# Optimization experiments

Measured on AMD Instinct MI355X. Metric: run time of the kernel, lower is better.

Reference implementation:

```python
import jax, jax.numpy as jnp
import numpy as np

B, L, C, H = 2, 4096, 512, 8
DH = C // H


def setup_inputs() -> dict:
    key = jax.random.key(0)
    ks = jax.random.split(key, 6)
    s = 1.0 / np.sqrt(C)
    return {
        "x": jax.random.normal(ks[0], (B, L, C), dtype=jnp.float32),
        "Wq": jax.random.normal(ks[1], (C, C), dtype=jnp.float32) * s,
        "Wk": jax.random.normal(ks[2], (C, C), dtype=jnp.float32) * s,
        "Wv": jax.random.normal(ks[3], (C, C), dtype=jnp.float32) * s,
        "Wo": jax.random.normal(ks[4], (C, C), dtype=jnp.float32) * s,
        "bo": jnp.zeros((C,), dtype=jnp.float32),
    }


def reference(x, Wq, Wk, Wv, Wo, bo):
    # x: [B, L, C]; split heads -> [B, H, L, Dh]
    def heads(t):
        return t.reshape(B, L, H, DH).transpose(0, 2, 1, 3)

    q = heads(x @ Wq)
    k = heads(x @ Wk)
    v = heads(x @ Wv)
    scale = 1.0 / np.sqrt(DH)
    scores = jnp.einsum("bhqd,bhkd->bhqk", q, k) * scale  # [B,H,L,L]
    w = jax.nn.softmax(scores, axis=-1)  # dropout_rate=0.0 -> identity
    att = jnp.einsum("bhqk,bhkd->bhqd", w, v)  # [B,H,L,Dh]
    att = att.transpose(0, 2, 1, 3).reshape(B, L, C)
    return att @ Wo + bo
```

## Files before the change

kernel.cpp:

```cpp
#include <hip/hip_runtime.h>
#include <hip/hip_bf16.h>

typedef __hip_bfloat16 bh;
typedef __attribute__((ext_vector_type(8))) __bf16 bf16x8;
typedef __attribute__((ext_vector_type(4))) float f32x4;
typedef __attribute__((ext_vector_type(4))) int i32x4;
typedef __attribute__((ext_vector_type(4))) short s16x4;

#define NB 2
#define NL 4096
#define NC 512
#define NH 8
#define NDH 64
#define NM (NB * NL)
#define LOG2E 1.4426950408889634f
#define KVBLK 8192

static __device__ __forceinline__ f32x4 mfma_bf16(bf16x8 a, bf16x8 b, f32x4 c) {
    return __builtin_amdgcn_mfma_f32_16x16x32_bf16(a, b, c, 0, 0, 0);
}
static __device__ __forceinline__ f32x4 mfma16(s16x4 a, s16x4 b, f32x4 c) {
    return __builtin_amdgcn_mfma_f32_16x16x16bf16_1k(a, b, c, 0, 0, 0);
}

static __device__ __forceinline__ void st_bf4(bh* dst, float a, float b, float c, float d) {
    bh tmp[4] = {__float2bfloat16(a), __float2bfloat16(b),
                 __float2bfloat16(c), __float2bfloat16(d)};
    *(s16x4*)dst = *(const s16x4*)tmp;
}
static __device__ __forceinline__ s16x4 pk_bf4(float a, float b, float c, float d) {
    bh tmp[4] = {__float2bfloat16(a), __float2bfloat16(b),
                 __float2bfloat16(c), __float2bfloat16(d)};
    return *(const s16x4*)tmp;
}

static __device__ __forceinline__ void gload16(const bh* g, bh* l) {
    __builtin_amdgcn_global_load_lds(
        (const __attribute__((address_space(1))) void*)g,
        (__attribute__((address_space(3))) void*)l,
        16, 0, 0);
}

__global__ __launch_bounds__(256, 2)
void prep(const float* __restrict__ x,
          const float* __restrict__ Wq, const float* __restrict__ Wk,
          const float* __restrict__ Wv, const float* __restrict__ Wo,
          bh* __restrict__ xf, bh* __restrict__ Wf)
{
    const int t = threadIdx.x;
    const int wave = t >> 6, lane = t & 63;
    const int quad = lane >> 4, c16 = lane & 15;

    if (blockIdx.z < 8) {
        __shared__ __align__(16) bh T[64][72];
        const int m64 = blockIdx.x, k64 = blockIdx.z;
        #pragma unroll
        for (int rep = 0; rep < 4; rep++) {
            int li = t + rep * 256;
            int r = li >> 4, c4 = (li & 15) * 4;
            float4 f = *(const float4*)&x[(size_t)(m64 * 64 + r) * 512 + k64 * 64 + c4];
            st_bf4(&T[r][c4], f.x, f.y, f.z, f.w);
        }
        __syncthreads();
        #pragma unroll
        for (int kcl = 0; kcl < 2; kcl++) {
            i32x4 v = *(const i32x4*)&T[wave * 16 + c16][kcl * 32 + quad * 8];
            size_t addr = ((size_t)(m64 * 4 + wave) * 16 + (k64 * 2 + kcl)) * 512 + lane * 8;
            *(i32x4*)&xf[addr] = v;
        }
    } else {
        if (blockIdx.x >= 64) return;
        int task = blockIdx.x * 4 + wave;
        int z = task >> 6, nt = (task >> 3) & 7, k0i = task & 7;
        const float* W = (z == 0) ? Wq : (z == 1) ? Wk : (z == 2) ? Wv : Wo;
        bh* dst = Wf + (((size_t)z * 8 + nt) * 8 + k0i) * 4096;
        #pragma unroll
        for (int kc = 0; kc < 2; kc++)
            #pragma unroll
            for (int fn = 0; fn < 4; fn++) {
                bh tmp[8];
                #pragma unroll
                for (int j = 0; j < 8; j++)
                    tmp[j] = __float2bfloat16(
                        W[(size_t)(k0i * 64 + kc * 32 + quad * 8 + j) * 512
                          + nt * 64 + fn * 16 + c16]);
                *(i32x4*)&dst[(kc * 4 + fn) * 512 + lane * 8] = *(const i32x4*)tmp;
            }
    }
}

__global__ __launch_bounds__(256, 2)
void qkv_gemm(const bh* __restrict__ xf, const bh* __restrict__ Wf,
              bh* __restrict__ Qb, bh* __restrict__ KVf)
{
    __shared__ __align__(16) bh smem[2][20480];

    const int t = threadIdx.x;
    const int wave = t >> 6, lane = t & 63;
    const int quad = lane >> 4, c16 = lane & 15;
    const int m0 = blockIdx.x * 128;
    const int nt = blockIdx.y;
    const int m16b = m0 >> 4;

    f32x4 acc[3][2][4];
    for (int z = 0; z < 3; z++)
        for (int a = 0; a < 2; a++)
            for (int b = 0; b < 4; b++)
                for (int u = 0; u < 4; u++) acc[z][a][b][u] = 0.0f;

    auto stage = [&](int k0i, int buf) {
        bh* Xl = &smem[buf][0];
        bh* Wl = &smem[buf][8192];
        #pragma unroll
        for (int r = 0; r < 4; r++) {
            int f = wave * 4 + r;
            const bh* src = xf + ((size_t)(m16b + (f >> 1)) * 16 + k0i * 2 + (f & 1)) * 512
                          + lane * 8;
            gload16(src, &Xl[f * 512 + lane * 8]);
        }
        #pragma unroll
        for (int z = 0; z < 3; z++) {
            const bh* wz = Wf + (((size_t)z * 8 + nt) * 8 + k0i) * 4096;
            #pragma unroll
            for (int r = 0; r < 2; r++) {
                int off = (wave * 2 + r) * 512 + lane * 8;
                gload16(wz + off, &Wl[z * 4096 + off]);
            }
        }
    };

    stage(0, 0);
    for (int k0i = 0; k0i < 8; k0i++) {
        const int buf = k0i & 1;
        __syncthreads();
        if (k0i < 7) stage(k0i + 1, buf ^ 1);
        const bh* Xl = &smem[buf][0];
        const bh* Wl = &smem[buf][8192];
        #pragma unroll
        for (int kc = 0; kc < 2; kc++) {
            bf16x8 af0 = *(const bf16x8*)&Xl[((wave * 2 + 0) * 2 + kc) * 512 + lane * 8];
            bf16x8 af1 = *(const bf16x8*)&Xl[((wave * 2 + 1) * 2 + kc) * 512 + lane * 8];
            #pragma unroll
            for (int z = 0; z < 3; z++)
                #pragma unroll
                for (int fn = 0; fn < 4; fn++) {
                    bf16x8 bf = *(const bf16x8*)&Wl[z * 4096 + (kc * 4 + fn) * 512 + lane * 8];
                    acc[z][0][fn] = mfma_bf16(af0, bf, acc[z][0][fn]);
                    acc[z][1][fn] = mfma_bf16(af1, bf, acc[z][1][fn]);
                }
        }
        __syncthreads();
    }

    const int h = nt;
    const int b = m0 >> 12;
    const int l0 = m0 & 4095;
    const int bh_i = b * NH + h;
    const int kt0 = l0 >> 6;

    {
        bh* Tq = &smem[0][0];
        #pragma unroll
        for (int fm = 0; fm < 2; fm++)
            #pragma unroll
            for (int i = 0; i < 4; i++) {
                int ll = wave * 32 + fm * 16 + quad * 4 + i;
                #pragma unroll
                for (int fn = 0; fn < 4; fn++)
                    Tq[ll * 68 + fn * 16 + c16] =
                        __float2bfloat16(acc[0][fm][fn][i] * 0.125f);
            }
        __syncthreads();
        int l = t >> 1, half = t & 1;
        bh* dst = Qb + ((size_t)bh_i * NL + l0 + l) * NDH + half * 32;
        const bh* src = &Tq[l * 68 + half * 32];
        #pragma unroll
        for (int r = 0; r < 4; r++)
            *(i32x4*)(dst + r * 8) = *(const i32x4*)(src + r * 8);
        __syncthreads();
    }

    {
        bh* Tk = &smem[0][0];
        #pragma unroll
        for (int fm = 0; fm < 2; fm++)
            #pragma unroll
            for (int i = 0; i < 4; i++) {
                int ll = wave * 32 + fm * 16 + quad * 4 + i;
                int ktl = ll >> 6, l64 = ll & 63;
                int fk = l64 >> 4, c16t = l64 & 15;
                #pragma unroll
                for (int fn = 0; fn < 4; fn++) {
                    int d = fn * 16 + c16;
                    int kc = d >> 5, qt = (d >> 3) & 3, j = d & 7;
                    Tk[ktl * 4096 + (fk * 2 + kc) * 512 + (qt * 16 + c16t) * 8 + j] =
                        __float2bfloat16(acc[1][fm][fn][i] * LOG2E);
                }
            }
        __syncthreads();
        int idx = t * 32;
        int ktl = idx >> 12, wi = idx & 4095;
        bh* dst = KVf + (size_t)(bh_i * 64 + kt0 + ktl) * KVBLK + wi;
        #pragma unroll
        for (int r = 0; r < 4; r++)
            *(i32x4*)(dst + r * 8) = *(const i32x4*)&Tk[idx + r * 8];
    }

    #pragma unroll
    for (int fm = 0; fm < 2; fm++) {
        int fkv = (wave * 2 + fm) & 3;
        int ktv = kt0 + (wave >> 1);
        #pragma unroll
        for (int fn = 0; fn < 4; fn++) {
            size_t addr = (size_t)(bh_i * 64 + ktv) * KVBLK + 4096
                        + (size_t)(fn * 4 + fkv) * 256 + (quad * 16 + c16) * 4;
            st_bf4(&KVf[addr], acc[2][fm][fn][0], acc[2][fm][fn][1],
                               acc[2][fm][fn][2], acc[2][fm][fn][3]);
        }
    }
}

__global__ __launch_bounds__(512, 4)
void flash_attn(const bh* __restrict__ Qb, const bh* __restrict__ KVf,
                bh* __restrict__ attb)
{
    __shared__ __align__(16) bh SF[2][2][KVBLK];

    const int t = threadIdx.x;
    const int wave = t >> 6, lane = t & 63;
    const int group = wave >> 2, w4 = wave & 3;
    const int quad = lane >> 4, c16 = lane & 15;
    const int bh_idx = blockIdx.y;
    const int q0 = blockIdx.x * 128;

    const bh* Qp  = Qb + (size_t)bh_idx * NL * NDH;
    const bh* KVp = KVf + (size_t)bh_idx * 64 * KVBLK;

    bf16x8 qf[2][2];
    #pragma unroll
    for (int fq = 0; fq < 2; fq++)
        #pragma unroll
        for (int kc = 0; kc < 2; kc++)
            qf[fq][kc] = *(const bf16x8*)
                &Qp[(size_t)(q0 + w4 * 32 + fq * 16 + c16) * NDH + kc * 32 + quad * 8];

    f32x4 ot[4][2];
    float lsum[2] = {0.0f, 0.0f};
    for (int a = 0; a < 4; a++)
        for (int fq = 0; fq < 2; fq++)
            for (int u = 0; u < 4; u++) ot[a][fq][u] = 0.0f;
    const f32x4 z4 = {0.0f, 0.0f, 0.0f, 0.0f};

    auto stage = [&](int i, int buf) {
        int kt = 2 * i + group;
        #pragma unroll
        for (int r = 0; r < 4; r++) {
            int off = (w4 * 4 + r) * 512 + lane * 8;
            gload16(KVp + (size_t)kt * KVBLK + off, &SF[group][buf][off]);
        }
    };

    stage(0, 0);
    for (int i = 0; i < 32; i++) {
        const int buf = i & 1;
        __syncthreads();
        if (i < 31) stage(i + 1, buf ^ 1);
        const bh* sf = &SF[group][buf][0];

        f32x4 s[4][2];
        #pragma unroll
        for (int fk = 0; fk < 4; fk++) {
            bf16x8 kf0 = *(const bf16x8*)&sf[(fk * 2 + 0) * 512 + lane * 8];
            s[fk][0] = mfma_bf16(kf0, qf[0][0], z4);
            s[fk][1] = mfma_bf16(kf0, qf[1][0], z4);
        }
        #pragma unroll
        for (int fk = 0; fk < 4; fk++) {
            bf16x8 kf1 = *(const bf16x8*)&sf[(fk * 2 + 1) * 512 + lane * 8];
            s[fk][0] = mfma_bf16(kf1, qf[0][1], s[fk][0]);
            s[fk][1] = mfma_bf16(kf1, qf[1][1], s[fk][1]);
        }

        s16x4 vt[4][4];
        #pragma unroll
        for (int fn = 0; fn < 4; fn++)
            #pragma unroll
            for (int fk = 0; fk < 4; fk++)
                vt[fn][fk] = *(const s16x4*)&sf[4096 + (fn * 4 + fk) * 256 + lane * 4];

        s16x4 pf[4][2];
        float rs0 = 0.0f, rs1 = 0.0f;
        #pragma unroll
        for (int fk = 0; fk < 4; fk++) {
            float a0 = __builtin_amdgcn_exp2f(s[fk][0][0]);
            float a1 = __builtin_amdgcn_exp2f(s[fk][0][1]);
            float a2 = __builtin_amdgcn_exp2f(s[fk][0][2]);
            float a3 = __builtin_amdgcn_exp2f(s[fk][0][3]);
            rs0 += (a0 + a1) + (a2 + a3);
            pf[fk][0] = pk_bf4(a0, a1, a2, a3);
            float b0 = __builtin_amdgcn_exp2f(s[fk][1][0]);
            float b1 = __builtin_amdgcn_exp2f(s[fk][1][1]);
            float b2 = __builtin_amdgcn_exp2f(s[fk][1][2]);
            float b3 = __builtin_amdgcn_exp2f(s[fk][1][3]);
            rs1 += (b0 + b1) + (b2 + b3);
            pf[fk][1] = pk_bf4(b0, b1, b2, b3);
        }
        lsum[0] += rs0;
        lsum[1] += rs1;

        #pragma unroll
        for (int fk = 0; fk < 4; fk++)
            #pragma unroll
            for (int fn = 0; fn < 4; fn++) {
                ot[fn][0] = mfma16(vt[fn][fk], pf[fk][0], ot[fn][0]);
                ot[fn][1] = mfma16(vt[fn][fk], pf[fk][1], ot[fn][1]);
            }
    }

    #pragma unroll
    for (int fq = 0; fq < 2; fq++) {
        lsum[fq] += __shfl_xor(lsum[fq], 16);
        lsum[fq] += __shfl_xor(lsum[fq], 32);
    }

    float* Ocmb = (float*)&SF[0][0][0];
    float* Lcmb = Ocmb + 128 * 64;
    __syncthreads();
    if (group == 1) {
        #pragma unroll
        for (int fq = 0; fq < 2; fq++) {
            int q = w4 * 32 + fq * 16 + c16;
            #pragma unroll
            for (int fn = 0; fn < 4; fn++)
                *(f32x4*)&Ocmb[q * 64 + fn * 16 + quad * 4] = ot[fn][fq];
            if (quad == 0) Lcmb[q] = lsum[fq];
        }
    }
    __syncthreads();
    if (group == 0) {
        const int b = bh_idx >> 3, h = bh_idx & 7;
        const int mbase16 = (b * NL + q0) >> 4;
        #pragma unroll
        for (int fq = 0; fq < 2; fq++) {
            int q = w4 * 32 + fq * 16 + c16;
            float inv = 1.0f / (lsum[fq] + Lcmb[q]);
            int m16 = mbase16 + w4 * 2 + fq;
            #pragma unroll
            for (int fn = 0; fn < 4; fn++) {
                f32x4 o2 = *(const f32x4*)&Ocmb[q * 64 + fn * 16 + quad * 4];
                size_t addr = ((size_t)m16 * 16 + h * 2 + (fn >> 1)) * 512
                            + (size_t)(((fn & 1) * 2 + (quad >> 1)) * 16 + c16) * 8
                            + (quad & 1) * 4;
                st_bf4(&attb[addr],
                       (ot[fn][fq][0] + o2[0]) * inv, (ot[fn][fq][1] + o2[1]) * inv,
                       (ot[fn][fq][2] + o2[2]) * inv, (ot[fn][fq][3] + o2[3]) * inv);
            }
        }
    }
}

__global__ __launch_bounds__(256, 2)
void out_gemm(const bh* __restrict__ Af, const bh* __restrict__ Wf,
              const float* __restrict__ bo, float* __restrict__ out)
{
    __shared__ __align__(16) bh smem[2][12288];

    const int t = threadIdx.x;
    const int wave = t >> 6, lane = t & 63;
    const int quad = lane >> 4, c16 = lane & 15;
    const int m0 = blockIdx.x * 128;
    const int nt = blockIdx.y;
    const int n0 = nt * 64;
    const int m16b = m0 >> 4;

    f32x4 acc[2][4];
    for (int a = 0; a < 2; a++)
        for (int b = 0; b < 4; b++)
            for (int u = 0; u < 4; u++) acc[a][b][u] = 0.0f;

    auto stage = [&](int k0i, int buf) {
        bh* Xl = &smem[buf][0];
        bh* Wl = &smem[buf][8192];
        #pragma unroll
        for (int r = 0; r < 4; r++) {
            int f = wave * 4 + r;
            const bh* src = Af + ((size_t)(m16b + (f >> 1)) * 16 + k0i * 2 + (f & 1)) * 512
                          + lane * 8;
            gload16(src, &Xl[f * 512 + lane * 8]);
        }
        const bh* wz = Wf + (((size_t)3 * 8 + nt) * 8 + k0i) * 4096;
        #pragma unroll
        for (int r = 0; r < 2; r++) {
            int off = (wave * 2 + r) * 512 + lane * 8;
            gload16(wz + off, &Wl[off]);
        }
    };

    stage(0, 0);
    for (int k0i = 0; k0i < 8; k0i++) {
        const int buf = k0i & 1;
        __syncthreads();
        if (k0i < 7) stage(k0i + 1, buf ^ 1);
        const bh* Xl = &smem[buf][0];
        const bh* Wl = &smem[buf][8192];
        #pragma unroll
        for (int kc = 0; kc < 2; kc++) {
            bf16x8 af0 = *(const bf16x8*)&Xl[((wave * 2 + 0) * 2 + kc) * 512 + lane * 8];
            bf16x8 af1 = *(const bf16x8*)&Xl[((wave * 2 + 1) * 2 + kc) * 512 + lane * 8];
            #pragma unroll
            for (int fn = 0; fn < 4; fn++) {
                bf16x8 bf = *(const bf16x8*)&Wl[(kc * 4 + fn) * 512 + lane * 8];
                acc[0][fn] = mfma_bf16(af0, bf, acc[0][fn]);
                acc[1][fn] = mfma_bf16(af1, bf, acc[1][fn]);
            }
        }
        __syncthreads();
    }

    #pragma unroll
    for (int fm = 0; fm < 2; fm++)
        #pragma unroll
        for (int i = 0; i < 4; i++) {
            int mr = m0 + wave * 32 + fm * 16 + quad * 4 + i;
            #pragma unroll
            for (int fn = 0; fn < 4; fn++) {
                int cn = n0 + fn * 16 + c16;
                out[(size_t)mr * 512 + cn] = acc[fm][fn][i] + bo[cn];
            }
        }
}

extern "C" void kernel_launch(void* const* d_in, const int* in_sizes, int n_in,
                              void* d_out, int out_size, void* d_ws, size_t ws_size,
                              hipStream_t stream)
{
    const float* x  = (const float*)d_in[0];
    const float* Wq = (const float*)d_in[1];
    const float* Wk = (const float*)d_in[2];
    const float* Wv = (const float*)d_in[3];
    const float* Wo = (const float*)d_in[4];
    const float* bo = (const float*)d_in[5];
    float* out = (float*)d_out;

    const size_t mat = (size_t)NM * NC;
    bh* Qb   = (bh*)d_ws;
    bh* KVf  = Qb + mat;
    bh* attb = KVf + 2 * mat;
    bh* Wf   = attb + mat;
    bh* xf   = Wf + 4 * 8 * 8 * 4096;

    prep      <<<dim3(128, 1, 9),         256, 0, stream>>>(x, Wq, Wk, Wv, Wo, xf, Wf);
    qkv_gemm  <<<dim3(NM / 128, NC / 64), 256, 0, stream>>>(xf, Wf, Qb, KVf);
    flash_attn<<<dim3(NL / 128, NB * NH), 512, 0, stream>>>(Qb, KVf, attb);
    out_gemm  <<<dim3(NM / 128, NC / 64), 256, 0, stream>>>(attb, Wf, bo, out);
}
```

Measured before the change: 186.9 us.

## Halve GEMM M-tile to 64 and single-buffer weights for higher occupancy

Both the QKV and output projection GEMMs now use 64-row M tiles, so each wave computes one 16-row fragment instead of two. The grid doubles and launch bounds rise to 4 blocks per CU. Weight tiles move to a single LDS buffer that is reloaded after the compute barrier, while X stays double-buffered. This lowers LDS and register use to fit more blocks and give more parallelism, but weight loads are now serialized with compute, each B fragment is reused less, and weight tiles are fetched from global memory twice as often.

New measurement: 188.8 us. No clear change (+1.0%).

```diff
diff --git a/kernel.cpp b/kernel.cpp
--- a/kernel.cpp
+++ b/kernel.cpp
@@ -89,35 +89,33 @@
     }
 }
 
-__global__ __launch_bounds__(256, 2)
+__global__ __launch_bounds__(256, 4)
 void qkv_gemm(const bh* __restrict__ xf, const bh* __restrict__ Wf,
               bh* __restrict__ Qb, bh* __restrict__ KVf)
 {
-    __shared__ __align__(16) bh smem[2][20480];
+    __shared__ __align__(16) bh Xl[2][4096];
+    __shared__ __align__(16) bh Wl[3 * 4096];
 
     const int t = threadIdx.x;
     const int wave = t >> 6, lane = t & 63;
     const int quad = lane >> 4, c16 = lane & 15;
-    const int m0 = blockIdx.x * 128;
+    const int m0 = blockIdx.x * 64;
     const int nt = blockIdx.y;
-    const int m16b = m0 >> 4;
-
-    f32x4 acc[3][2][4];
+    const int m16 = (m0 >> 4) + wave;
+
+    f32x4 acc[3][4];
     for (int z = 0; z < 3; z++)
-        for (int a = 0; a < 2; a++)
-            for (int b = 0; b < 4; b++)
-                for (int u = 0; u < 4; u++) acc[z][a][b][u] = 0.0f;
-
-    auto stage = [&](int k0i, int buf) {
-        bh* Xl = &smem[buf][0];
-        bh* Wl = &smem[buf][8192];
-        #pragma unroll
-        for (int r = 0; r < 4; r++) {
-            int f = wave * 4 + r;
-            const bh* src = xf + ((size_t)(m16b + (f >> 1)) * 16 + k0i * 2 + (f & 1)) * 512
-                          + lane * 8;
-            gload16(src, &Xl[f * 512 + lane * 8]);
-        }
+        for (int b = 0; b < 4; b++)
+            for (int u = 0; u < 4; u++) acc[z][b][u] = 0.0f;
+
+    auto stageX = [&](int k0i, int buf) {
+        #pragma unroll
+        for (int kcl = 0; kcl < 2; kcl++) {
+            const bh* src = xf + ((size_t)m16 * 16 + k0i * 2 + kcl) * 512 + lane * 8;
+            gload16(src, &Xl[buf][wave * 1024 + kcl * 512 + lane * 8]);
+        }
+    };
+    auto stageW = [&](int k0i) {
         #pragma unroll
         for (int z = 0; z < 3; z++) {
             const bh* wz = Wf + (((size_t)z * 8 + nt) * 8 + k0i) * 4096;
@@ -129,27 +127,25 @@
         }
     };
 
-    stage(0, 0);
+    stageX(0, 0);
+    stageW(0);
     for (int k0i = 0; k0i < 8; k0i++) {
         const int buf = k0i & 1;
         __syncthreads();
-        if (k0i < 7) stage(k0i + 1, buf ^ 1);
-        const bh* Xl = &smem[buf][0];
-        const bh* Wl = &smem[buf][8192];
+        if (k0i < 7) stageX(k0i + 1, buf ^ 1);
         #pragma unroll
         for (int kc = 0; kc < 2; kc++) {
-            bf16x8 af0 = *(const bf16x8*)&Xl[((wave * 2 + 0) * 2 + kc) * 512 + lane * 8];
-            bf16x8 af1 = *(const bf16x8*)&Xl[((wave * 2 + 1) * 2 + kc) * 512 + lane * 8];
+            bf16x8 af = *(const bf16x8*)&Xl[buf][wave * 1024 + kc * 512 + lane * 8];
             #pragma unroll
             for (int z = 0; z < 3; z++)
                 #pragma unroll
                 for (int fn = 0; fn < 4; fn++) {
                     bf16x8 bf = *(const bf16x8*)&Wl[z * 4096 + (kc * 4 + fn) * 512 + lane * 8];
-                    acc[z][0][fn] = mfma_bf16(af0, bf, acc[z][0][fn]);
-                    acc[z][1][fn] = mfma_bf16(af1, bf, acc[z][1][fn]);
+                    acc[z][fn] = mfma_bf16(af, bf, acc[z][fn]);
                 }
         }
         __syncthreads();
+        if (k0i < 7) stageW(k0i + 1);
     }
 
     const int h = nt;
@@ -159,64 +155,50 @@
     const int kt0 = l0 >> 6;
 
     {
-        bh* Tq = &smem[0][0];
-        #pragma unroll
-        for (int fm = 0; fm < 2; fm++)
-            #pragma unroll
-            for (int i = 0; i < 4; i++) {
-                int ll = wave * 32 + fm * 16 + quad * 4 + i;
-                #pragma unroll
-                for (int fn = 0; fn < 4; fn++)
-                    Tq[ll * 68 + fn * 16 + c16] =
-                        __float2bfloat16(acc[0][fm][fn][i] * 0.125f);
-            }
-        __syncthreads();
-        int l = t >> 1, half = t & 1;
-        bh* dst = Qb + ((size_t)bh_i * NL + l0 + l) * NDH + half * 32;
-        const bh* src = &Tq[l * 68 + half * 32];
-        #pragma unroll
-        for (int r = 0; r < 4; r++)
-            *(i32x4*)(dst + r * 8) = *(const i32x4*)(src + r * 8);
+        bh* Tq = &Wl[0];
+        #pragma unroll
+        for (int i = 0; i < 4; i++) {
+            int ll = wave * 16 + quad * 4 + i;
+            #pragma unroll
+            for (int fn = 0; fn < 4; fn++)
+                Tq[ll * 68 + fn * 16 + c16] =
+                    __float2bfloat16(acc[0][fn][i] * 0.125f);
+        }
+        __syncthreads();
+        int l = t >> 2, qtr = t & 3;
+        bh* dst = Qb + ((size_t)bh_i * NL + l0 + l) * NDH + qtr * 16;
+        const bh* src = &Tq[l * 68 + qtr * 16];
+        *(i32x4*)(dst + 0) = *(const i32x4*)(src + 0);
+        *(i32x4*)(dst + 8) = *(const i32x4*)(src + 8);
         __syncthreads();
     }
 
     {
-        bh* Tk = &smem[0][0];
-        #pragma unroll
-        for (int fm = 0; fm < 2; fm++)
-            #pragma unroll
-            for (int i = 0; i < 4; i++) {
-                int ll = wave * 32 + fm * 16 + quad * 4 + i;
-                int ktl = ll >> 6, l64 = ll & 63;
-                int fk = l64 >> 4, c16t = l64 & 15;
-                #pragma unroll
-                for (int fn = 0; fn < 4; fn++) {
-                    int d = fn * 16 + c16;
-                    int kc = d >> 5, qt = (d >> 3) & 3, j = d & 7;
-                    Tk[ktl * 4096 + (fk * 2 + kc) * 512 + (qt * 16 + c16t) * 8 + j] =
-                        __float2bfloat16(acc[1][fm][fn][i] * LOG2E);
-                }
-            }
-        __syncthreads();
-        int idx = t * 32;
-        int ktl = idx >> 12, wi = idx & 4095;
-        bh* dst = KVf + (size_t)(bh_i * 64 + kt0 + ktl) * KVBLK + wi;
-        #pragma unroll
-        for (int r = 0; r < 4; r++)
-            *(i32x4*)(dst + r * 8) = *(const i32x4*)&Tk[idx + r * 8];
+        bh* Tk = &Wl[0];
+        #pragma unroll
+        for (int i = 0; i < 4; i++) {
+            int ll = wave * 16 + quad * 4 + i;
+            int fk = wave, c16t = ll & 15;
+            #pragma unroll
+            for (int fn = 0; fn < 4; fn++) {
+                int d = fn * 16 + c16;
+                int kc = d >> 5, qt = (d >> 3) & 3, j = d & 7;
+                Tk[(fk * 2 + kc) * 512 + (qt * 16 + c16t) * 8 + j] =
+                    __float2bfloat16(acc[1][fn][i] * LOG2E);
+            }
+        }
+        __syncthreads();
+        bh* dst = KVf + (size_t)(bh_i * 64 + kt0) * KVBLK + t * 16;
+        *(i32x4*)(dst + 0) = *(const i32x4*)&Tk[t * 16 + 0];
+        *(i32x4*)(dst + 8) = *(const i32x4*)&Tk[t * 16 + 8];
     }
 
     #pragma unroll
-    for (int fm = 0; fm < 2; fm++) {
-        int fkv = (wave * 2 + fm) & 3;
-        int ktv = kt0 + (wave >> 1);
-        #pragma unroll
-        for (int fn = 0; fn < 4; fn++) {
-            size_t addr = (size_t)(bh_i * 64 + ktv) * KVBLK + 4096
-                        + (size_t)(fn * 4 + fkv) * 256 + (quad * 16 + c16) * 4;
-            st_bf4(&KVf[addr], acc[2][fm][fn][0], acc[2][fm][fn][1],
-                               acc[2][fm][fn][2], acc[2][fm][fn][3]);
-        }
+    for (int fn = 0; fn < 4; fn++) {
+        size_t addr = (size_t)(bh_i * 64 + kt0) * KVBLK + 4096
+                    + (size_t)(fn * 4 + wave) * 256 + (quad * 16 + c16) * 4;
+        st_bf4(&KVf[addr], acc[2][fn][0], acc[2][fn][1],
+                           acc[2][fn][2], acc[2][fn][3]);
     }
 }
 
@@ -359,35 +341,33 @@
     }
 }
 
-__global__ __launch_bounds__(256, 2)
+__global__ __launch_bounds__(256, 4)
 void out_gemm(const bh* __restrict__ Af, const bh* __restrict__ Wf,
               const float* __restrict__ bo, float* __restrict__ out)
 {
-    __shared__ __align__(16) bh smem[2][12288];
+    __shared__ __align__(16) bh Xl[2][4096];
+    __shared__ __align__(16) bh Wl[4096];
 
     const int t = threadIdx.x;
     const int wave = t >> 6, lane = t & 63;
     const int quad = lane >> 4, c16 = lane & 15;
-    const int m0 = blockIdx.x * 128;
+    const int m0 = blockIdx.x * 64;
     const int nt = blockIdx.y;
     const int n0 = nt * 64;
-    const int m16b = m0 >> 4;
-
-    f32x4 acc[2][4];
-    for (int a = 0; a < 2; a++)
-        for (int b = 0; b < 4; b++)
-            for (int u = 0; u < 4; u++) acc[a][b][u] = 0.0f;
-
-    auto stage = [&](int k0i, int buf) {
-        bh* Xl = &smem[buf][0];
-        bh* Wl = &smem[buf][8192];
-        #pragma unroll
-        for (int r = 0; r < 4; r++) {
-            int f = wave * 4 + r;
-            const bh* src = Af + ((size_t)(m16b + (f >> 1)) * 16 + k0i * 2 + (f & 1)) * 512
-                          + lane * 8;
-            gload16(src, &Xl[f * 512 + lane * 8]);
-        }
+    const int m16 = (m0 >> 4) + wave;
+
+    f32x4 acc[4];
+    for (int b = 0; b < 4; b++)
+        for (int u = 0; u < 4; u++) acc[b][u] = 0.0f;
+
+    auto stageX = [&](int k0i, int buf) {
+        #pragma unroll
+        for (int kcl = 0; kcl < 2; kcl++) {
+            const bh* src = Af + ((size_t)m16 * 16 + k0i * 2 + kcl) * 512 + lane * 8;
+            gload16(src, &Xl[buf][wave * 1024 + kcl * 512 + lane * 8]);
+        }
+    };
+    auto stageW = [&](int k0i) {
         const bh* wz = Wf + (((size_t)3 * 8 + nt) * 8 + k0i) * 4096;
         #pragma unroll
         for (int r = 0; r < 2; r++) {
@@ -396,38 +376,34 @@
         }
     };
 
-    stage(0, 0);
+    stageX(0, 0);
+    stageW(0);
     for (int k0i = 0; k0i < 8; k0i++) {
         const int buf = k0i & 1;
         __syncthreads();
-        if (k0i < 7) stage(k0i + 1, buf ^ 1);
-        const bh* Xl = &smem[buf][0];
-        const bh* Wl = &smem[buf][8192];
+        if (k0i < 7) stageX(k0i + 1, buf ^ 1);
         #pragma unroll
         for (int kc = 0; kc < 2; kc++) {
-            bf16x8 af0 = *(const bf16x8*)&Xl[((wave * 2 + 0) * 2 + kc) * 512 + lane * 8];
-            bf16x8 af1 = *(const bf16x8*)&Xl[((wave * 2 + 1) * 2 + kc) * 512 + lane * 8];
+            bf16x8 af = *(const bf16x8*)&Xl[buf][wave * 1024 + kc * 512 + lane * 8];
             #pragma unroll
             for (int fn = 0; fn < 4; fn++) {
                 bf16x8 bf = *(const bf16x8*)&Wl[(kc * 4 + fn) * 512 + lane * 8];
-                acc[0][fn] = mfma_bf16(af0, bf, acc[0][fn]);
-                acc[1][fn] = mfma_bf16(af1, bf, acc[1][fn]);
-            }
-        }
-        __syncthreads();
+                acc[fn] = mfma_bf16(af, bf, acc[fn]);
+            }
+        }
+        __syncthreads();
+        if (k0i < 7) stageW(k0i + 1);
     }
 
     #pragma unroll
-    for (int fm = 0; fm < 2; fm++)
-        #pragma unroll
-        for (int i = 0; i < 4; i++) {
-            int mr = m0 + wave * 32 + fm * 16 + quad * 4 + i;
-            #pragma unroll
-            for (int fn = 0; fn < 4; fn++) {
-                int cn = n0 + fn * 16 + c16;
-                out[(size_t)mr * 512 + cn] = acc[fm][fn][i] + bo[cn];
-            }
-        }
+    for (int i = 0; i < 4; i++) {
+        int mr = m0 + wave * 16 + quad * 4 + i;
+        #pragma unroll
+        for (int fn = 0; fn < 4; fn++) {
+            int cn = n0 + fn * 16 + c16;
+            out[(size_t)mr * 512 + cn] = acc[fn][i] + bo[cn];
+        }
+    }
 }
 
 extern "C" void kernel_launch(void* const* d_in, const int* in_sizes, int n_in,
@@ -450,7 +426,7 @@
     bh* xf   = Wf + 4 * 8 * 8 * 4096;
 
     prep      <<<dim3(128, 1, 9),         256, 0, stream>>>(x, Wq, Wk, Wv, Wo, xf, Wf);
-    qkv_gemm  <<<dim3(NM / 128, NC / 64), 256, 0, stream>>>(xf, Wf, Qb, KVf);
+    qkv_gemm  <<<dim3(NM / 64, NC / 64),  256, 0, stream>>>(xf, Wf, Qb, KVf);
     flash_attn<<<dim3(NL / 128, NB * NH), 512, 0, stream>>>(Qb, KVf, attb);
-    out_gemm  <<<dim3(NM / 128, NC / 64), 256, 0, stream>>>(attb, Wf, bo, out);
-}
+    out_gemm  <<<dim3(NM / 64, NC / 64),  256, 0, stream>>>(attb, Wf, bo, out);
+}
```
